# Optimization experiments

Measured on AMD Instinct MI355X. Metric: run time of the kernel, lower is better.

Reference implementation:

```python
import jax, jax.numpy as jnp
import numpy as np

B, N, E = 4, 1024, 16
S = 4  # num species
AH = PH = 64  # hidden dims


def _mlp(x, W0, b0, W1, b1, W2, b2):
    h = jax.nn.silu(x @ W0 + b0)
    h = jax.nn.silu(h @ W1 + b1)
    return h @ W2 + b2  # [..., 1]


def setup_inputs() -> dict:
    key = jax.random.key(0)
    ks = jax.random.split(key, 20)
    scale = 0.1
    inp = {
        "positions": jax.random.normal(ks[0], (B, N, 2), jnp.float32),
        "species": jax.random.randint(ks[1], (B, N), 0, S, jnp.int32),
        "electric_field": jax.random.normal(ks[2], (B, 2), jnp.float32),
        "embed": jax.random.normal(ks[3], (S, E), jnp.float32) * scale,
        "aW0": jax.random.normal(ks[4], (2 + 2 + 1 + E, AH), jnp.float32) * scale,
        "ab0": jax.random.normal(ks[5], (AH,), jnp.float32) * scale,
        "aW1": jax.random.normal(ks[6], (AH, AH), jnp.float32) * scale,
        "ab1": jax.random.normal(ks[7], (AH,), jnp.float32) * scale,
        "aW2": jax.random.normal(ks[8], (AH, 1), jnp.float32) * scale,
        "ab2": jax.random.normal(ks[9], (1,), jnp.float32) * scale,
        "pW0": jax.random.normal(ks[10], (2 + 1 + 1 + 1 + 2 * E, PH), jnp.float32) * scale,
        "pb0": jax.random.normal(ks[11], (PH,), jnp.float32) * scale,
        "pW1": jax.random.normal(ks[12], (PH, PH), jnp.float32) * scale,
        "pb1": jax.random.normal(ks[13], (PH,), jnp.float32) * scale,
        "pW2": jax.random.normal(ks[14], (PH, 1), jnp.float32) * scale,
        "pb2": jax.random.normal(ks[15], (1,), jnp.float32) * scale,
    }
    return inp


def reference(positions, species, electric_field, embed,
              aW0, ab0, aW1, ab1, aW2, ab2,
              pW0, pb0, pW1, pb1, pW2, pb2):
    num_atoms = positions.shape[1]
    cp = positions - positions.mean(axis=1, keepdims=True)         # [B,N,2]
    semb = embed[species]                                          # [B,N,E]
    e_norm = jnp.linalg.norm(electric_field, axis=-1, keepdims=True)  # [B,1]

    # atom channel
    atom_field = jnp.broadcast_to(electric_field[:, None, :], (cp.shape[0], num_atoms, 2))
    atom_enorm = jnp.broadcast_to(e_norm[:, None, :], (cp.shape[0], num_atoms, 1))
    atom_feat = jnp.concatenate([cp, atom_field, atom_enorm, semb], axis=-1)
    atom_energy = _mlp(atom_feat, aW0, ab0, aW1, ab1, aW2, ab2)[..., 0].sum(axis=1)

    # pair channel: all i<j pairs, fully vectorized
    i_idx, j_idx = jnp.triu_indices(num_atoms, k=1)                # [P]
    rij = cp[:, i_idx, :] - cp[:, j_idx, :]                        # [B,P,2]
    dij = jnp.linalg.norm(rij, axis=-1, keepdims=True)             # [B,P,1]
    uij = rij / jnp.maximum(dij, 1e-12)
    e_dot_u = jnp.sum(electric_field[:, None, :] * uij, axis=-1, keepdims=True)
    pair_enorm = jnp.broadcast_to(e_norm[:, None, :], dij.shape)
    pair_feat = jnp.concatenate(
        [rij, dij, e_dot_u, pair_enorm, semb[:, i_idx, :], semb[:, j_idx, :]], axis=-1)
    pair_energy = _mlp(pair_feat, pW0, pb0, pW1, pb1, pW2, pb2)[..., 0].sum(axis=1)

    return atom_energy + pair_energy
```

## Files before the change

### kernel.cpp

```cpp
#include <hip/hip_runtime.h>

#define NA 1024
#define NBATCH 4
#define NPAIR 523776
#define PAIR_TILES 2046
#define PAIR_BLOCKS 512
#define GRID_X 513

#define WS_MEAN 0
#define WS_W0P  64
#define WS_W0A  4160
#define WS_W1P  8256
#define WS_W1A  16448

typedef _Float16 half8 __attribute__((ext_vector_type(8)));
typedef float float4v __attribute__((ext_vector_type(4)));

__device__ __forceinline__ float silu_f(float x) {
    return x * __builtin_amdgcn_rcpf(1.0f + __expf(-x));
}

__device__ __forceinline__ uint32_t pkf16(float a, float b) {
    union { _Float16 h[2]; uint32_t u; } x;
    x.h[0] = (_Float16)a; x.h[1] = (_Float16)b;
    return x.u;
}

__global__ void prep_kernel(const float* __restrict__ positions,
                            const float* __restrict__ embed,
                            const float* __restrict__ aW0,
                            const float* __restrict__ aW1,
                            const float* __restrict__ ab2,
                            const float* __restrict__ pW0,
                            const float* __restrict__ pW1,
                            const float* __restrict__ pb2,
                            char* __restrict__ ws,
                            float* __restrict__ out) {
    const int tid = threadIdx.x;
    if (blockIdx.x < 4) {
        const int b = blockIdx.x;
        const float2* pos = (const float2*)positions + b * NA;
        float sx = 0.f, sy = 0.f;
        for (int t = tid; t < NA; t += 256) {
            float2 p = pos[t];
            sx += p.x; sy += p.y;
        }
#pragma unroll
        for (int off = 32; off > 0; off >>= 1) {
            sx += __shfl_down(sx, off);
            sy += __shfl_down(sy, off);
        }
        __shared__ float rxs[4], rys[4];
        const int w = tid >> 6, lane = tid & 63;
        if (lane == 0) { rxs[w] = sx; rys[w] = sy; }
        __syncthreads();
        if (tid == 0) {
            float* meanws = (float*)(ws + WS_MEAN);
            meanws[b * 2 + 0] = (rxs[0] + rxs[1] + rxs[2] + rxs[3]) * (1.f / NA);
            meanws[b * 2 + 1] = (rys[0] + rys[1] + rys[2] + rys[3]) * (1.f / NA);
            out[b] = (float)NPAIR * pb2[0] + (float)NA * ab2[0];
        }
        return;
    }

    _Float16* w0p = (_Float16*)(ws + WS_W0P);
    _Float16* w0a = (_Float16*)(ws + WS_W0A);
    _Float16* w1p = (_Float16*)(ws + WS_W1P);
    _Float16* w1a = (_Float16*)(ws + WS_W1A);

    for (int idx = tid; idx < 2048; idx += 256) {
        const int j = idx & 7, lane = (idx >> 3) & 63, nt = idx >> 9;
        const int k = ((lane >> 4) << 3) + j;
        const int col = nt * 16 + (lane & 15);
        float vp = 0.f, va = 0.f;
        if (k < 5) {
            vp = pW0[k * 64 + col];
            va = aW0[k * 64 + col];
        } else if (k >= 6 && k <= 9) {
            const int s = k - 6;
            float accp = 0.f, acca = 0.f;
#pragma unroll
            for (int e = 0; e < 16; e++) {
                float em = embed[s * 16 + e];
                accp += em * pW0[(5 + e) * 64 + col];
                acca += em * aW0[(5 + e) * 64 + col];
            }
            vp = accp; va = acca;
        } else if (k >= 10 && k <= 13) {
            const int s = k - 10;
            float accp = 0.f;
#pragma unroll
            for (int e = 0; e < 16; e++)
                accp += embed[s * 16 + e] * pW0[(21 + e) * 64 + col];
            vp = accp; va = 0.f;
        }
        w0p[idx] = (_Float16)vp;
        w0a[idx] = (_Float16)va;
    }
    for (int idx = tid; idx < 4096; idx += 256) {
        const int j = idx & 7, lane = (idx >> 3) & 63;
        const int ks = (idx >> 9) & 1, nt = idx >> 10;
        const int k = ks * 32 + ((lane >> 4) << 3) + j;
        const int col = nt * 16 + (lane & 15);
        w1p[idx] = (_Float16)pW1[k * 64 + col];
        w1a[idx] = (_Float16)aW1[k * 64 + col];
    }
}

__global__ __launch_bounds__(256, 4) void mlp_kernel(
    const float* __restrict__ positions,
    const int*   __restrict__ species,
    const float* __restrict__ efield,
    const float* __restrict__ ab0, const float* __restrict__ ab1,
    const float* __restrict__ aW2,
    const float* __restrict__ pb0, const float* __restrict__ pb1,
    const float* __restrict__ pW2,
    const char*  __restrict__ ws,
    float* __restrict__ out)
{
    const int b    = blockIdx.y;
    const int bx   = blockIdx.x;
    const bool is_atom = (bx == PAIR_BLOCKS);
    const int tid  = threadIdx.x;
    const int lane = tid & 63;
    const int wv   = tid >> 6;
    const int n16  = lane & 15;
    const int quad = lane >> 4;

    __shared__ __attribute__((aligned(16))) _Float16 Hbuf[4][64][72];
    _Float16 (*rows)[72] = Hbuf[wv];

    const _Float16* w0w = (const _Float16*)(ws + (is_atom ? WS_W0A : WS_W0P));
    const _Float16* w1w = (const _Float16*)(ws + (is_atom ? WS_W1A : WS_W1P));
    half8 w0f[4], w1f[4][2];
#pragma unroll
    for (int nt = 0; nt < 4; nt++)
        w0f[nt] = *(const half8*)(w0w + (nt * 64 + lane) * 8);
#pragma unroll
    for (int nt = 0; nt < 4; nt++)
#pragma unroll
        for (int ks = 0; ks < 2; ks++)
            w1f[nt][ks] = *(const half8*)(w1w + ((nt * 2 + ks) * 64 + lane) * 8);

    const float* B0 = is_atom ? ab0 : pb0;
    const float* B1 = is_atom ? ab1 : pb1;
    const float* W2 = is_atom ? aW2 : pW2;
    float b0v[4], b1v[4], w2v[4];
#pragma unroll
    for (int nt = 0; nt < 4; nt++) {
        b0v[nt] = B0[nt * 16 + n16];
        b1v[nt] = B1[nt * 16 + n16];
        w2v[nt] = W2[nt * 16 + n16];
    }

    const float Ex = efield[b * 2 + 0];
    const float Ey = efield[b * 2 + 1];
    const float enorm = sqrtf(Ex * Ex + Ey * Ey);
    const float* meanws = (const float*)(ws + WS_MEAN);

    const int my_tiles = is_atom ? 4 : ((bx < PAIR_TILES - 3 * PAIR_BLOCKS) ? 4 : 3);

    float energy = 0.f;
    for (int t = 0; t < my_tiles; ++t) {
        float f0, f1, f2, f3;
        uint64_t ohi, ohj;
        if (!is_atom) {
            const int tile = bx + t * PAIR_BLOCKS;
            const int p = tile * 256 + tid;
            float Df = (float)(2047 * 2047 - 8 * p);
            int i = (int)((2047.0f - sqrtf(Df)) * 0.5f);
            i = i < 0 ? 0 : (i > 1022 ? 1022 : i);
            while (i * (2047 - i) / 2 > p) --i;
            while ((i + 1) * (2046 - i) / 2 <= p) ++i;
            const int j = p - i * (2047 - i) / 2 + i + 1;
            const float2* pos = (const float2*)positions + b * NA;
            float2 pi = pos[i], pj = pos[j];
            f0 = pi.x - pj.x; f1 = pi.y - pj.y;
            f2 = sqrtf(f0 * f0 + f1 * f1);
            float inv = __builtin_amdgcn_rcpf(fmaxf(f2, 1e-12f));
            f3 = (Ex * f0 + Ey * f1) * inv;
            ohi = 0x3C00ull << (species[b * NA + i] * 16);
            ohj = 0x3C00ull << (species[b * NA + j] * 16);
        } else {
            const int n = t * 256 + tid;
            float2 pn = ((const float2*)positions)[b * NA + n];
            f0 = pn.x - meanws[b * 2 + 0];
            f1 = pn.y - meanws[b * 2 + 1];
            f2 = Ex; f3 = Ey;
            ohi = 0x3C00ull << (species[b * NA + n] * 16);
            ohj = 0;
        }
        int4* dst = (int4*)&rows[lane][0];
        int4 lo, hi;
        lo.x = (int)pkf16(f0, f1);
        lo.y = (int)pkf16(f2, f3);
        lo.z = (int)pkf16(enorm, 0.f);
        lo.w = (int)(uint32_t)ohi;
        hi.x = (int)(uint32_t)(ohi >> 32);
        hi.y = (int)(uint32_t)ohj;
        hi.z = (int)(uint32_t)(ohj >> 32);
        hi.w = 0;
        dst[0] = lo;
        dst[1] = hi;
        dst[2] = make_int4(0, 0, 0, 0);
        dst[3] = make_int4(0, 0, 0, 0);

#pragma unroll
        for (int mt = 0; mt < 4; mt++) {
            const _Float16* arow = &rows[mt * 16 + n16][0];
            half8 a = *(const half8*)(arow + quad * 8);

            float4v acc[4];
#pragma unroll
            for (int nt = 0; nt < 4; nt++) {
                float4v c = {b0v[nt], b0v[nt], b0v[nt], b0v[nt]};
                acc[nt] = __builtin_amdgcn_mfma_f32_16x16x32_f16(a, w0f[nt], c, 0, 0, 0);
            }
#pragma unroll
            for (int nt = 0; nt < 4; nt++)
#pragma unroll
                for (int r = 0; r < 4; r++)
                    rows[mt * 16 + quad * 4 + r][nt * 16 + n16] =
                        (_Float16)silu_f(acc[nt][r]);

            const _Float16* hrow = &rows[mt * 16 + n16][0];
            half8 h0 = *(const half8*)(hrow + quad * 8);
            half8 h1 = *(const half8*)(hrow + 32 + quad * 8);
            float4v acc2[4];
#pragma unroll
            for (int nt = 0; nt < 4; nt++) {
                float4v c = {b1v[nt], b1v[nt], b1v[nt], b1v[nt]};
                c = __builtin_amdgcn_mfma_f32_16x16x32_f16(h0, w1f[nt][0], c, 0, 0, 0);
                c = __builtin_amdgcn_mfma_f32_16x16x32_f16(h1, w1f[nt][1], c, 0, 0, 0);
                acc2[nt] = c;
            }
#pragma unroll
            for (int nt = 0; nt < 4; nt++)
#pragma unroll
                for (int r = 0; r < 4; r++)
                    energy += silu_f(acc2[nt][r]) * w2v[nt];
        }
    }

#pragma unroll
    for (int off = 32; off > 0; off >>= 1)
        energy += __shfl_down(energy, off);
    __shared__ float wsum[4];
    if (lane == 0) wsum[wv] = energy;
    __syncthreads();
    if (tid == 0)
        atomicAdd(&out[b], wsum[0] + wsum[1] + wsum[2] + wsum[3]);
}

extern "C" void kernel_launch(void* const* d_in, const int* in_sizes, int n_in,
                              void* d_out, int out_size, void* d_ws, size_t ws_size,
                              hipStream_t stream) {
    const float* positions = (const float*)d_in[0];
    const int*   species   = (const int*)  d_in[1];
    const float* efield    = (const float*)d_in[2];
    const float* embed     = (const float*)d_in[3];
    const float* aW0 = (const float*)d_in[4];
    const float* ab0 = (const float*)d_in[5];
    const float* aW1 = (const float*)d_in[6];
    const float* ab1 = (const float*)d_in[7];
    const float* aW2 = (const float*)d_in[8];
    const float* ab2 = (const float*)d_in[9];
    const float* pW0 = (const float*)d_in[10];
    const float* pb0 = (const float*)d_in[11];
    const float* pW1 = (const float*)d_in[12];
    const float* pb1 = (const float*)d_in[13];
    const float* pW2 = (const float*)d_in[14];
    const float* pb2 = (const float*)d_in[15];
    float* outp = (float*)d_out;
    char*  ws   = (char*)d_ws;

    prep_kernel<<<dim3(5), dim3(256), 0, stream>>>(
        positions, embed, aW0, aW1, ab2, pW0, pW1, pb2, ws, outp);
    mlp_kernel<<<dim3(GRID_X, NBATCH), dim3(256), 0, stream>>>(
        positions, species, efield,
        ab0, ab1, aW2, pb0, pb1, pW2,
        ws, outp);
}
```

Measured before the change: 169.0 us.

## Transpose MFMA operands to keep hidden layer in registers, fold bias into W0

Swaps the MFMA operand order so layer-1 outputs land in a register layout that feeds layer 2 directly. This removes the LDS write and read round-trip of the 64x64 hidden tile, and the W1 fragment packing is permuted to match. The layer-0 bias is folded into W0 as an extra input row set to 1.0, and the zero padding of the feature rows is written once outside the loop, which shrinks shared memory. The risk is subtle layout mismatches in the fragment permutation.

```diff
diff --git a/kernel.cpp b/kernel.cpp
--- a/kernel.cpp
+++ b/kernel.cpp
@@ -29,9 +29,11 @@
 __global__ void prep_kernel(const float* __restrict__ positions,
                             const float* __restrict__ embed,
                             const float* __restrict__ aW0,
+                            const float* __restrict__ ab0,
                             const float* __restrict__ aW1,
                             const float* __restrict__ ab2,
                             const float* __restrict__ pW0,
+                            const float* __restrict__ pb0,
                             const float* __restrict__ pW1,
                             const float* __restrict__ pb2,
                             char* __restrict__ ws,
@@ -76,6 +78,9 @@
         if (k < 5) {
             vp = pW0[k * 64 + col];
             va = aW0[k * 64 + col];
+        } else if (k == 5) {
+            vp = pb0[col];
+            va = ab0[col];
         } else if (k >= 6 && k <= 9) {
             const int s = k - 6;
             float accp = 0.f, acca = 0.f;
@@ -100,7 +105,9 @@
     for (int idx = tid; idx < 4096; idx += 256) {
         const int j = idx & 7, lane = (idx >> 3) & 63;
         const int ks = (idx >> 9) & 1, nt = idx >> 10;
-        const int k = ks * 32 + ((lane >> 4) << 3) + j;
+        const int q = lane >> 4;
+        const int m = (j < 4) ? (4 * q + j) : (16 + 4 * q + (j - 4));
+        const int k = ks * 32 + m;
         const int col = nt * 16 + (lane & 15);
         w1p[idx] = (_Float16)pW1[k * 64 + col];
         w1a[idx] = (_Float16)aW1[k * 64 + col];
@@ -111,10 +118,8 @@
     const float* __restrict__ positions,
     const int*   __restrict__ species,
     const float* __restrict__ efield,
-    const float* __restrict__ ab0, const float* __restrict__ ab1,
-    const float* __restrict__ aW2,
-    const float* __restrict__ pb0, const float* __restrict__ pb1,
-    const float* __restrict__ pW2,
+    const float* __restrict__ ab1, const float* __restrict__ aW2,
+    const float* __restrict__ pb1, const float* __restrict__ pW2,
     const char*  __restrict__ ws,
     float* __restrict__ out)
 {
@@ -127,8 +132,8 @@
     const int n16  = lane & 15;
     const int quad = lane >> 4;
 
-    __shared__ __attribute__((aligned(16))) _Float16 Hbuf[4][64][72];
-    _Float16 (*rows)[72] = Hbuf[wv];
+    __shared__ __attribute__((aligned(16))) _Float16 Xbuf[4][64][40];
+    _Float16 (*rows)[40] = Xbuf[wv];
 
     const _Float16* w0w = (const _Float16*)(ws + (is_atom ? WS_W0A : WS_W0P));
     const _Float16* w1w = (const _Float16*)(ws + (is_atom ? WS_W1A : WS_W1P));
@@ -142,16 +147,17 @@
         for (int ks = 0; ks < 2; ks++)
             w1f[nt][ks] = *(const half8*)(w1w + ((nt * 2 + ks) * 64 + lane) * 8);
 
-    const float* B0 = is_atom ? ab0 : pb0;
     const float* B1 = is_atom ? ab1 : pb1;
     const float* W2 = is_atom ? aW2 : pW2;
-    float b0v[4], b1v[4], w2v[4];
+    float4v b1q[4], w2q[4];
 #pragma unroll
     for (int nt = 0; nt < 4; nt++) {
-        b0v[nt] = B0[nt * 16 + n16];
-        b1v[nt] = B1[nt * 16 + n16];
-        w2v[nt] = W2[nt * 16 + n16];
-    }
+        b1q[nt] = *(const float4v*)(B1 + nt * 16 + quad * 4);
+        w2q[nt] = *(const float4v*)(W2 + nt * 16 + quad * 4);
+    }
+
+    *(int4*)&rows[lane][16] = make_int4(0, 0, 0, 0);
+    *(int4*)&rows[lane][24] = make_int4(0, 0, 0, 0);
 
     const float Ex = efield[b * 2 + 0];
     const float Ey = efield[b * 2 + 1];
@@ -194,7 +200,7 @@
         int4 lo, hi;
         lo.x = (int)pkf16(f0, f1);
         lo.y = (int)pkf16(f2, f3);
-        lo.z = (int)pkf16(enorm, 0.f);
+        lo.z = (int)pkf16(enorm, 1.0f);
         lo.w = (int)(uint32_t)ohi;
         hi.x = (int)(uint32_t)(ohi >> 32);
         hi.y = (int)(uint32_t)ohj;
@@ -202,43 +208,35 @@
         hi.w = 0;
         dst[0] = lo;
         dst[1] = hi;
-        dst[2] = make_int4(0, 0, 0, 0);
-        dst[3] = make_int4(0, 0, 0, 0);
 
 #pragma unroll
         for (int mt = 0; mt < 4; mt++) {
-            const _Float16* arow = &rows[mt * 16 + n16][0];
-            half8 a = *(const half8*)(arow + quad * 8);
+            half8 xf = *(const half8*)(&rows[mt * 16 + n16][quad * 8]);
 
             float4v acc[4];
 #pragma unroll
             for (int nt = 0; nt < 4; nt++) {
-                float4v c = {b0v[nt], b0v[nt], b0v[nt], b0v[nt]};
-                acc[nt] = __builtin_amdgcn_mfma_f32_16x16x32_f16(a, w0f[nt], c, 0, 0, 0);
-            }
-#pragma unroll
-            for (int nt = 0; nt < 4; nt++)
+                float4v z = {0.f, 0.f, 0.f, 0.f};
+                acc[nt] = __builtin_amdgcn_mfma_f32_16x16x32_f16(w0f[nt], xf, z, 0, 0, 0);
+            }
+            half8 h0, h1;
+#pragma unroll
+            for (int r = 0; r < 4; r++) {
+                h0[r]     = (_Float16)silu_f(acc[0][r]);
+                h0[4 + r] = (_Float16)silu_f(acc[1][r]);
+                h1[r]     = (_Float16)silu_f(acc[2][r]);
+                h1[4 + r] = (_Float16)silu_f(acc[3][r]);
+            }
+
+#pragma unroll
+            for (int nt = 0; nt < 4; nt++) {
+                float4v c = b1q[nt];
+                c = __builtin_amdgcn_mfma_f32_16x16x32_f16(w1f[nt][0], h0, c, 0, 0, 0);
+                c = __builtin_amdgcn_mfma_f32_16x16x32_f16(w1f[nt][1], h1, c, 0, 0, 0);
 #pragma unroll
                 for (int r = 0; r < 4; r++)
-                    rows[mt * 16 + quad * 4 + r][nt * 16 + n16] =
-                        (_Float16)silu_f(acc[nt][r]);
-
-            const _Float16* hrow = &rows[mt * 16 + n16][0];
-            half8 h0 = *(const half8*)(hrow + quad * 8);
-            half8 h1 = *(const half8*)(hrow + 32 + quad * 8);
-            float4v acc2[4];
-#pragma unroll
-            for (int nt = 0; nt < 4; nt++) {
-                float4v c = {b1v[nt], b1v[nt], b1v[nt], b1v[nt]};
-                c = __builtin_amdgcn_mfma_f32_16x16x32_f16(h0, w1f[nt][0], c, 0, 0, 0);
-                c = __builtin_amdgcn_mfma_f32_16x16x32_f16(h1, w1f[nt][1], c, 0, 0, 0);
-                acc2[nt] = c;
-            }
-#pragma unroll
-            for (int nt = 0; nt < 4; nt++)
-#pragma unroll
-                for (int r = 0; r < 4; r++)
-                    energy += silu_f(acc2[nt][r]) * w2v[nt];
+                    energy += silu_f(c[r]) * w2q[nt][r];
+            }
         }
     }
 
@@ -275,9 +273,9 @@
     char*  ws   = (char*)d_ws;
 
     prep_kernel<<<dim3(5), dim3(256), 0, stream>>>(
-        positions, embed, aW0, aW1, ab2, pW0, pW1, pb2, ws, outp);
+        positions, embed, aW0, ab0, aW1, ab2, pW0, pb0, pW1, pb2, ws, outp);
     mlp_kernel<<<dim3(GRID_X, NBATCH), dim3(256), 0, stream>>>(
         positions, species, efield,
-        ab0, ab1, aW2, pb0, pb1, pW2,
+        ab1, aW2, pb1, pW2,
         ws, outp);
 }
```

After: 169.2 us. About the same (+0.1%).
